# Kernel tuning notes

Hardware: AMD Instinct MI355X
Metric: run time of the kernel (lower is better)

Reference implementation:

```python
import jax, jax.numpy as jnp
import numpy as np

NUM_CLASSES = 151
EMBED = 200
HID = 512
OBJ_DIM = 4096
POS = 128
OBJ_IN = OBJ_DIM + EMBED + POS          # 4424
DEC_IN = HID + OBJ_IN                    # 4936
EDGE_IN = EMBED + HID + OBJ_DIM          # 4808
BN_EPS = 1e-5


def lstm_scan(xs, Wi, Wh, b):
    # xs: [T, D]; sequential chain LSTM (with_chain=True, chain_style='LSTM')
    H = Wh.shape[0]
    h0 = jnp.zeros((H,), xs.dtype)
    c0 = jnp.zeros((H,), xs.dtype)
    pre = xs @ Wi + b  # [T, 4H] hoist input projection out of the scan

    def step(carry, pt):
        h, c = carry
        g = pt + h @ Wh
        i, f, gg, o = jnp.split(g, 4)
        c = jax.nn.sigmoid(f) * c + jax.nn.sigmoid(i) * jnp.tanh(gg)
        h = jax.nn.sigmoid(o) * jnp.tanh(c)
        return (h, c), h

    _, hs = jax.lax.scan(step, (h0, c0), pre)
    return hs  # [T, H]


def setup_inputs() -> dict:
    key = jax.random.key(0)
    ks = jax.random.split(key, 24)
    s = 0.02
    N, B = 2048, 16
    inp = {
        "x": jax.random.normal(ks[0], (N, OBJ_DIM), jnp.float32),
        "obj_dists_in": jax.random.uniform(ks[1], (N, NUM_CLASSES), jnp.float32),
        "box_info": jax.random.uniform(ks[2], (N, 9), jnp.float32),
        "virtual_obj": jax.random.uniform(ks[3], (B, OBJ_IN), jnp.float32),
        "virtual_edge": jax.random.uniform(ks[4], (B, EDGE_IN), jnp.float32),
        # embeddings (GloVe-initialized in the original)
        "embed1": jax.random.normal(ks[5], (NUM_CLASSES, EMBED), jnp.float32) * s,
        "embed2": jax.random.normal(ks[6], (NUM_CLASSES, EMBED), jnp.float32) * s,
        # pos_embed MLP: Linear(9,32) -> BN(32) -> Linear(32,128) -> ReLU
        "pos_W1": jax.random.normal(ks[7], (9, 32), jnp.float32) * s,
        "pos_b1": jnp.zeros((32,), jnp.float32),
        "bn_gamma": jnp.ones((32,), jnp.float32),
        "bn_beta": jnp.zeros((32,), jnp.float32),
        "bn_mean": jnp.zeros((32,), jnp.float32),
        "bn_var": jnp.ones((32,), jnp.float32),
        "pos_W2": jax.random.normal(ks[8], (32, POS), jnp.float32) * s,
        "pos_b2": jnp.zeros((POS,), jnp.float32),
        # object context LSTM
        "obj_Wi": jax.random.normal(ks[9], (OBJ_IN, 4 * HID), jnp.float32) * s,
        "obj_Wh": jax.random.normal(ks[10], (HID, 4 * HID), jnp.float32) * s,
        "obj_b": jnp.zeros((4 * HID,), jnp.float32),
        # decoder tree-LSTM
        "dec_Wi": jax.random.normal(ks[11], (DEC_IN, 4 * HID), jnp.float32) * s,
        "dec_Wh": jax.random.normal(ks[12], (HID, 4 * HID), jnp.float32) * s,
        "dec_b": jnp.zeros((4 * HID,), jnp.float32),
        "out_W": jax.random.normal(ks[13], (HID, NUM_CLASSES), jnp.float32) * s,
        "out_b": jnp.zeros((NUM_CLASSES,), jnp.float32),
        # edge context LSTM
        "edge_Wi": jax.random.normal(ks[14], (EDGE_IN, 4 * HID), jnp.float32) * s,
        "edge_Wh": jax.random.normal(ks[15], (HID, 4 * HID), jnp.float32) * s,
        "edge_b": jnp.zeros((4 * HID,), jnp.float32),
    }
    return inp


def reference(x, obj_dists_in, box_info, virtual_obj, virtual_edge,
              embed1, embed2,
              pos_W1, pos_b1, bn_gamma, bn_beta, bn_mean, bn_var, pos_W2, pos_b2,
              obj_Wi, obj_Wh, obj_b,
              dec_Wi, dec_Wh, dec_b, out_W, out_b,
              edge_Wi, edge_Wh, edge_b):
    N = x.shape[0]
    B = virtual_obj.shape[0]
    # soft label embedding (sgdet/sgcls path): dists @ embed1.weight
    obj_embed = obj_dists_in @ embed1                      # [N, EMBED]
    # pos_embed MLP (BatchNorm in eval mode with running stats)
    h = box_info @ pos_W1 + pos_b1
    h = (h - bn_mean) * jax.lax.rsqrt(bn_var + BN_EPS) * bn_gamma + bn_beta
    pos_embed = jax.nn.relu(h @ pos_W2 + pos_b2)           # [N, POS]
    obj_pre_rep = jnp.concatenate([x, obj_embed, pos_embed], axis=-1)  # [N, OBJ_IN]

    # obj_ctx: append one virtual node per tree, chain tree-LSTM over the forest
    feats = jnp.concatenate([obj_pre_rep, virtual_obj], axis=0)        # [N+B, OBJ_IN]
    encoder_rep_full = lstm_scan(feats, obj_Wi, obj_Wh, obj_b)         # [N+B, HID]

    # decoder tree-LSTM: per-node recurrence + linear classification
    decoder_inp = jnp.concatenate([feats, encoder_rep_full], axis=1)   # [N+B, DEC_IN]
    dec_h = lstm_scan(decoder_inp, dec_Wi, dec_Wh, dec_b)              # [N+B, HID]
    dists_full = dec_h @ out_W + out_b                                 # [N+B, C]
    obj_dist = dists_full[:N]                    # strip virtual nodes ([:-B])
    obj_pred = jnp.argmax(obj_dist, axis=-1)     # commitments

    encoder_rep = encoder_rep_full[:N]

    # edge context: embed2 lookup on predicted labels + chain LSTM
    obj_embed2 = embed2[obj_pred]                                      # [N, EMBED]
    obj_rel_rep = jnp.concatenate([obj_embed2, x, encoder_rep], axis=-1)  # [N, EDGE_IN]
    edge_feats = jnp.concatenate([obj_rel_rep, virtual_edge], axis=0)
    edge_ctx = lstm_scan(edge_feats, edge_Wi, edge_Wh, edge_b)[:N]     # [N, HID]

    return obj_dist, obj_pred, edge_ctx
```

## Files before the change

### kernel.cpp

```cpp
#include <hip/hip_runtime.h>
#include <cstdint>
#include <cstddef>

#define N_OBJ 2048
#define NUM_CLASSES 151
#define EMBED 200
#define HID 512
#define OBJ_DIM 4096
#define POS 128
#define OBJ_IN 4424
#define EDGE_IN 4808
#define G4 2048
#define TSTEPS 2048
#define SPIN_FUSED 12000
#define OUT_PRED 309248
#define OUT_EDGE 311296

typedef unsigned long long ull;

__global__ void init_sync_kernel(unsigned* p, long n) {
  long i = blockIdx.x * (long)blockDim.x + threadIdx.x;
  long stride = (long)gridDim.x * blockDim.x;
  for (; i < n; i += stride) p[i] = 0u;
}

__global__ void obj_embed2_kernel(const float* __restrict__ dists,
                                  const float* __restrict__ embed1,
                                  float* __restrict__ objemb) {
  int r = blockIdx.x;
  __shared__ float drow[NUM_CLASSES];
  for (int c = threadIdx.x; c < NUM_CLASSES; c += blockDim.x)
    drow[c] = dists[(size_t)r * NUM_CLASSES + c];
  __syncthreads();
  for (int j = threadIdx.x; j < EMBED; j += blockDim.x) {
    float s = 0.f;
    for (int k = 0; k < NUM_CLASSES; ++k)
      s = fmaf(drow[k], embed1[(size_t)k * EMBED + j], s);
    objemb[(size_t)r * EMBED + j] = s;
  }
}

__global__ void pos2_kernel(const float* __restrict__ box,
                            const float* __restrict__ W1, const float* __restrict__ b1,
                            const float* __restrict__ gamma, const float* __restrict__ beta,
                            const float* __restrict__ mean, const float* __restrict__ var,
                            const float* __restrict__ W2, const float* __restrict__ b2,
                            float* __restrict__ posemb) {
  int r = blockIdx.x;
  __shared__ float h[32];
  __shared__ float bx[9];
  if (threadIdx.x < 9) bx[threadIdx.x] = box[(size_t)r * 9 + threadIdx.x];
  __syncthreads();
  if (threadIdx.x < 32) {
    float s = b1[threadIdx.x];
    for (int k = 0; k < 9; ++k) s = fmaf(bx[k], W1[k * 32 + threadIdx.x], s);
    s = (s - mean[threadIdx.x]) * (1.f / sqrtf(var[threadIdx.x] + 1e-5f)) * gamma[threadIdx.x]
        + beta[threadIdx.x];
    h[threadIdx.x] = s;
  }
  __syncthreads();
  int j = threadIdx.x;
  if (j < POS) {
    float s = b2[j];
    for (int k = 0; k < 32; ++k) s = fmaf(h[k], W2[k * POS + j], s);
    posemb[(size_t)r * POS + j] = fmaxf(s, 0.f);
  }
}

template <int ACC>
__global__ __launch_bounds__(256)
void gemm_kernel(const float* __restrict__ A, int lda,
                 const float* __restrict__ B, int ldb,
                 const float* __restrict__ bias,
                 float* __restrict__ C, int ldc,
                 int M, int N, int K) {
  __shared__ __align__(16) float As[16][68];
  __shared__ __align__(16) float Bs[16][64];
  const int row0 = blockIdx.y * 64;
  const int col0 = blockIdx.x * 64;
  const int tid = threadIdx.x;
  const int tx = tid & 15, ty = tid >> 4;
  float acc[4][4] = {};

  for (int k0 = 0; k0 < K; k0 += 16) {
#pragma unroll
    for (int l = 0; l < 4; ++l) {
      int idx = tid + l * 256;
      int m = idx >> 4, kk = idx & 15;
      int gm = row0 + m, gk = k0 + kk;
      As[kk][m] = (gm < M && gk < K) ? A[(size_t)gm * lda + gk] : 0.f;
    }
#pragma unroll
    for (int l = 0; l < 4; ++l) {
      int idx = tid + l * 256;
      int kk = idx >> 6, n = idx & 63;
      int gk = k0 + kk, gn = col0 + n;
      Bs[kk][n] = (gk < K && gn < N) ? B[(size_t)gk * ldb + gn] : 0.f;
    }
    __syncthreads();
#pragma unroll
    for (int kk = 0; kk < 16; ++kk) {
      float4 a = *reinterpret_cast<const float4*>(&As[kk][ty * 4]);
      float4 b = *reinterpret_cast<const float4*>(&Bs[kk][tx * 4]);
      acc[0][0] = fmaf(a.x, b.x, acc[0][0]); acc[0][1] = fmaf(a.x, b.y, acc[0][1]);
      acc[0][2] = fmaf(a.x, b.z, acc[0][2]); acc[0][3] = fmaf(a.x, b.w, acc[0][3]);
      acc[1][0] = fmaf(a.y, b.x, acc[1][0]); acc[1][1] = fmaf(a.y, b.y, acc[1][1]);
      acc[1][2] = fmaf(a.y, b.z, acc[1][2]); acc[1][3] = fmaf(a.y, b.w, acc[1][3]);
      acc[2][0] = fmaf(a.z, b.x, acc[2][0]); acc[2][1] = fmaf(a.z, b.y, acc[2][1]);
      acc[2][2] = fmaf(a.z, b.z, acc[2][2]); acc[2][3] = fmaf(a.z, b.w, acc[2][3]);
      acc[3][0] = fmaf(a.w, b.x, acc[3][0]); acc[3][1] = fmaf(a.w, b.y, acc[3][1]);
      acc[3][2] = fmaf(a.w, b.z, acc[3][2]); acc[3][3] = fmaf(a.w, b.w, acc[3][3]);
    }
    __syncthreads();
  }
#pragma unroll
  for (int i = 0; i < 4; ++i) {
    int gm = row0 + ty * 4 + i;
    if (gm >= M) continue;
#pragma unroll
    for (int j = 0; j < 4; ++j) {
      int gn = col0 + tx * 4 + j;
      if (gn >= N) continue;
      size_t o = (size_t)gm * ldc + gn;
      if (ACC) C[o] += acc[i][j];
      else C[o] = acc[i][j] + (bias ? bias[gn] : 0.f);
    }
  }
}

__device__ __forceinline__ void rec8_body(
    int blk, const float* __restrict__ pre, const float* __restrict__ Wh,
    const float* __restrict__ Wi2, ull* hXown, const ull* encXc,
    const ull* predX, const float* __restrict__ embT, float* outEdge,
    float4 (*w4)[32][64], float* hl, int* shPred) {
  const int tid = threadIdx.x;
  const int wv = tid >> 6;
  const int l = tid & 63;
  const int o = l & 7;
  const int c = l >> 3;
  const int gq = c & 3;
  const int dl = c >> 2;
  const int dim = blk * 8 + 2 * wv + dl;
  const int colw = gq * HID + dim;
  {
    const float* srcW = (o < 4) ? (Wh + (size_t)(o * 128) * G4 + colw)
                                : (Wi2 + (size_t)((o - 4) * 128) * G4 + colw);
#pragma unroll 4
    for (int j4 = 0; j4 < 32; ++j4) {
      float4 t;
      t.x = srcW[(size_t)(4 * j4 + 0) * G4];
      t.y = srcW[(size_t)(4 * j4 + 1) * G4];
      t.z = srcW[(size_t)(4 * j4 + 2) * G4];
      t.w = srcW[(size_t)(4 * j4 + 3) * G4];
      w4[wv][j4][l] = t;
    }
  }
  for (int i = tid; i < 1056; i += 256) hl[i] = 0.f;
  __syncthreads();

  float creg = 0.f;
  bool dead = false;
  for (int s = 0; s < TSTEPS; ++s) {
    float pre_v = pre[(size_t)s * G4 + colw];
    if (wv == 0) {
      const ull* srcE = encXc + (size_t)s * HID + l * 8;
      const ull* srcH = hXown + (size_t)(s - 1) * HID + l * 8;
      ull pe[8], ph[8], pp = 0;
      if (!dead) {
        int tries = 0;
        for (;;) {
          unsigned tE = 0xFFFFFFFFu, tH = 0xFFFFFFFFu, tP = 0xFFFFFFFFu;
#pragma unroll
          for (int j = 0; j < 8; ++j) {
            pe[j] = __hip_atomic_load(srcE + j, __ATOMIC_RELAXED, __HIP_MEMORY_SCOPE_AGENT);
            tE = min(tE, (unsigned)(pe[j] >> 32));
          }
          if (s > 0) {
#pragma unroll
            for (int j = 0; j < 8; ++j) {
              ph[j] = __hip_atomic_load(srcH + j, __ATOMIC_RELAXED, __HIP_MEMORY_SCOPE_AGENT);
              tH = min(tH, (unsigned)(ph[j] >> 32));
            }
          }
          if (predX) {
            pp = __hip_atomic_load(predX + s, __ATOMIC_RELAXED, __HIP_MEMORY_SCOPE_AGENT);
            tP = (unsigned)(pp >> 32);
          }
          bool ok = (tE >= (unsigned)(s + 1)) && (s == 0 || tH >= (unsigned)s) &&
                    (!predX || tP >= (unsigned)(s + 1));
          if (__all((int)ok)) break;
          if (++tries > SPIN_FUSED) { dead = true; break; }
          __builtin_amdgcn_s_sleep(2);
        }
      }
      if (dead) {
#pragma unroll
        for (int j = 0; j < 8; ++j) { pe[j] = 0ull; ph[j] = 0ull; }
        pp = 0;
      }
      const int ppH = 8 * l + 4 * (l >> 4);
      const int ppE = 528 + ppH;
      if (s > 0) {
#pragma unroll
        for (int j = 0; j < 8; ++j) hl[ppH + j] = __uint_as_float((unsigned)ph[j]);
      }
#pragma unroll
      for (int j = 0; j < 8; ++j) hl[ppE + j] = __uint_as_float((unsigned)pe[j]);
      if (predX && l == 0) *shPred = (int)(unsigned)(pp & 0xFFFFFFFFull);
    }
    __syncthreads();

    float emb = 0.f;
    if (embT) emb = embT[(size_t)(*shPred) * G4 + colw];

    float a0 = 0.f, a1 = 0.f, a2 = 0.f, a3 = 0.f;
    const float* hseg = &hl[132 * o];
#pragma unroll
    for (int j4 = 0; j4 < 32; ++j4) {
      float4 w = w4[wv][j4][l];
      float4 h4 = *reinterpret_cast<const float4*>(&hseg[4 * j4]);
      a0 = fmaf(w.x, h4.x, a0); a1 = fmaf(w.y, h4.y, a1);
      a2 = fmaf(w.z, h4.z, a2); a3 = fmaf(w.w, h4.w, a3);
    }
    float acc = (a0 + a1) + (a2 + a3);
    acc += __shfl_xor(acc, 1);
    acc += __shfl_xor(acc, 2);
    acc += __shfl_xor(acc, 4);
    float full = acc + pre_v + emb;
    int gb = dl * 32;
    float vi = __shfl(full, gb), vf = __shfl(full, gb + 8);
    float vg = __shfl(full, gb + 16), vo = __shfl(full, gb + 24);
    float si = 1.f / (1.f + __expf(-vi));
    float sf = 1.f / (1.f + __expf(-vf));
    float so = 1.f / (1.f + __expf(-vo));
    creg = sf * creg + si * tanhf(vg);
    float h = so * tanhf(creg);
    if ((l & 31) == 0) {
      if (outEdge) outEdge[(size_t)s * HID + dim] = h;
      ull pvs = ((ull)(unsigned)(s + 1) << 32) | (unsigned)__float_as_uint(h);
      __hip_atomic_store(hXown + (size_t)s * HID + dim, pvs, __ATOMIC_RELAXED,
                         __HIP_MEMORY_SCOPE_AGENT);
    }
  }
}

__global__ __launch_bounds__(256, 1)
void fused_all_kernel(const float* __restrict__ preO, const float* __restrict__ objWh,
                      const float* __restrict__ preD, const float* __restrict__ decWh,
                      const float* __restrict__ decWi2,
                      const float* __restrict__ epre, const float* __restrict__ embT,
                      const float* __restrict__ edgeWh, const float* __restrict__ edgeWi2,
                      const float* __restrict__ outW, const float* __restrict__ outB,
                      ull* encX, ull* dechX, ull* edgeX, ull* predX,
                      float* out) {
  __shared__ float4 w4[4][32][64];
  __shared__ float hl[1056];
  __shared__ int shPred;
  const int bid = blockIdx.x;
  const int tid = threadIdx.x;
  const int wv = tid >> 6;
  const int l = tid & 63;

  if (bid < 32) {
    const int q = l >> 2, qt = l & 3, dq = q >> 2, gq = q & 3;
    const int d0w = bid * 16 + wv * 4;
    const int colw = gq * HID + d0w + dq;
    {
      const float* base = objWh + (size_t)(qt * 128) * G4 + colw;
#pragma unroll 4
      for (int j4 = 0; j4 < 32; ++j4) {
        float4 t;
        t.x = base[(size_t)(4 * j4 + 0) * G4];
        t.y = base[(size_t)(4 * j4 + 1) * G4];
        t.z = base[(size_t)(4 * j4 + 2) * G4];
        t.w = base[(size_t)(4 * j4 + 3) * G4];
        w4[wv][j4][l] = t;
      }
    }
    for (int i = tid; i < 532; i += 256) hl[i] = 0.f;
    __syncthreads();

    float creg = 0.f;
    bool dead = false;
    for (int s = 0; s < TSTEPS; ++s) {
      float pre_v = preO[(size_t)s * G4 + colw];
      if (s > 0) {
        if (wv == 0) {
          const ull* src = encX + (size_t)(s - 1) * HID + l * 8;
          ull pv[8];
          if (!dead) {
            int tries = 0;
            for (;;) {
              unsigned tmin = 0xFFFFFFFFu;
#pragma unroll
              for (int j = 0; j < 8; ++j) {
                pv[j] = __hip_atomic_load(src + j, __ATOMIC_RELAXED, __HIP_MEMORY_SCOPE_AGENT);
                tmin = min(tmin, (unsigned)(pv[j] >> 32));
              }
              if (__all((int)(tmin >= (unsigned)s))) break;
              if (++tries > SPIN_FUSED) { dead = true; break; }
              __builtin_amdgcn_s_sleep(2);
            }
          }
          if (dead) {
#pragma unroll
            for (int j = 0; j < 8; ++j) pv[j] = 0ull;
          }
          const int pp = 8 * l + 4 * (l >> 4);
#pragma unroll
          for (int j = 0; j < 8; ++j) hl[pp + j] = __uint_as_float((unsigned)pv[j]);
        }
        __syncthreads();
      }
      float a0 = 0.f, a1 = 0.f, a2 = 0.f, a3 = 0.f;
      const float* hseg = &hl[132 * qt];
#pragma unroll
      for (int j4 = 0; j4 < 32; ++j4) {
        float4 w = w4[wv][j4][l];
        float4 h4 = *reinterpret_cast<const float4*>(&hseg[4 * j4]);
        a0 = fmaf(w.x, h4.x, a0); a1 = fmaf(w.y, h4.y, a1);
        a2 = fmaf(w.z, h4.z, a2); a3 = fmaf(w.w, h4.w, a3);
      }
      float acc = (a0 + a1) + (a2 + a3);
      acc += __shfl_xor(acc, 1);
      acc += __shfl_xor(acc, 2);
      float full = acc + pre_v;
      int gbase = (l & 48) | (l & 3);
      float vi = __shfl(full, gbase), vf = __shfl(full, gbase | 4);
      float vg = __shfl(full, gbase | 8), vo = __shfl(full, gbase | 12);
      float si = 1.f / (1.f + __expf(-vi));
      float sf = 1.f / (1.f + __expf(-vf));
      float so = 1.f / (1.f + __expf(-vo));
      creg = sf * creg + si * tanhf(vg);
      float h = so * tanhf(creg);
      if ((l & 15) == 0) {
        int dim = d0w + (l >> 4);
        ull pvs = ((ull)(unsigned)(s + 1) << 32) | (unsigned)__float_as_uint(h);
        __hip_atomic_store(encX + (size_t)s * HID + dim, pvs, __ATOMIC_RELAXED,
                           __HIP_MEMORY_SCOPE_AGENT);
      }
    }
  } else if (bid < 96) {
    rec8_body(bid - 32, preD, decWh, decWi2, dechX, encX,
              nullptr, nullptr, nullptr, w4, hl, &shPred);
  } else if (bid < 112) {
    const int a = bid - 96;
    float* dh = hl;
    float* lg = hl + 512;
    bool dead = false;
    for (int r = a; r < TSTEPS; r += 16) {
      if (wv == 0) {
        const ull* src = dechX + (size_t)r * HID + l * 8;
        ull pv[8];
        if (!dead) {
          int tries = 0;
          for (;;) {
            unsigned tmin = 0xFFFFFFFFu;
#pragma unroll
            for (int j = 0; j < 8; ++j) {
              pv[j] = __hip_atomic_load(src + j, __ATOMIC_RELAXED, __HIP_MEMORY_SCOPE_AGENT);
              tmin = min(tmin, (unsigned)(pv[j] >> 32));
            }
            if (__all((int)(tmin >= (unsigned)(r + 1)))) break;
            if (++tries > SPIN_FUSED) { dead = true; break; }
            __builtin_amdgcn_s_sleep(2);
          }
        }
        if (dead) {
#pragma unroll
          for (int j = 0; j < 8; ++j) pv[j] = 0ull;
        }
#pragma unroll
        for (int j = 0; j < 8; ++j) dh[l * 8 + j] = __uint_as_float((unsigned)pv[j]);
      }
      __syncthreads();
      if (tid < NUM_CLASSES) {
        float s2 = outB[tid];
#pragma unroll 8
        for (int k = 0; k < HID; ++k)
          s2 = fmaf(dh[k], outW[(size_t)k * NUM_CLASSES + tid], s2);
        lg[tid] = s2;
        out[(size_t)r * NUM_CLASSES + tid] = s2;
      }
      __syncthreads();
      if (wv == 0) {
        float bv = -3.4e38f;
        int bi = NUM_CLASSES;
        for (int cc = l; cc < NUM_CLASSES; cc += 64) {
          float v = lg[cc];
          if (v > bv) { bv = v; bi = cc; }
        }
        for (int off = 32; off; off >>= 1) {
          float ov = __shfl_xor(bv, off);
          int oi = __shfl_xor(bi, off);
          if (ov > bv || (ov == bv && oi < bi)) { bv = ov; bi = oi; }
        }
        if (l == 0) {
          out[OUT_PRED + r] = (float)bi;
          ull pvs = ((ull)(unsigned)(r + 1) << 32) | (unsigned)bi;
          __hip_atomic_store(predX + r, pvs, __ATOMIC_RELAXED, __HIP_MEMORY_SCOPE_AGENT);
        }
      }
      __syncthreads();
    }
  } else {
    rec8_body(bid - 112, epre, edgeWh, edgeWi2, edgeX, encX,
              predX, embT, out + OUT_EDGE, w4, hl, &shPred);
  }
}

extern "C" void kernel_launch(void* const* d_in, const int* in_sizes, int n_in,
                              void* d_out, int out_size, void* d_ws, size_t ws_size,
                              hipStream_t stream) {
  const float* x        = (const float*)d_in[0];
  const float* odists   = (const float*)d_in[1];
  const float* box      = (const float*)d_in[2];
  const float* embed1   = (const float*)d_in[5];
  const float* embed2   = (const float*)d_in[6];
  const float* pos_W1   = (const float*)d_in[7];
  const float* pos_b1   = (const float*)d_in[8];
  const float* bn_gamma = (const float*)d_in[9];
  const float* bn_beta  = (const float*)d_in[10];
  const float* bn_mean  = (const float*)d_in[11];
  const float* bn_var   = (const float*)d_in[12];
  const float* pos_W2   = (const float*)d_in[13];
  const float* pos_b2   = (const float*)d_in[14];
  const float* obj_Wi   = (const float*)d_in[15];
  const float* obj_Wh   = (const float*)d_in[16];
  const float* obj_b    = (const float*)d_in[17];
  const float* dec_Wi   = (const float*)d_in[18];
  const float* dec_Wh   = (const float*)d_in[19];
  const float* dec_b    = (const float*)d_in[20];
  const float* out_W    = (const float*)d_in[21];
  const float* out_b    = (const float*)d_in[22];
  const float* edge_Wi  = (const float*)d_in[23];
  const float* edge_Wh  = (const float*)d_in[24];
  const float* edge_b   = (const float*)d_in[25];

  float* out = (float*)d_out;

  float* preO   = (float*)d_ws;
  float* preD   = preO + (size_t)TSTEPS * G4;
  float* epre   = preD + (size_t)TSTEPS * G4;
  float* objemb = epre + (size_t)TSTEPS * G4;
  float* posemb = objemb + (size_t)TSTEPS * EMBED;
  float* embT   = posemb + (size_t)TSTEPS * POS;
  ull* encX  = (ull*)(embT + (size_t)NUM_CLASSES * G4);
  ull* dechX = encX + (size_t)TSTEPS * HID;
  ull* edgeX = dechX + (size_t)TSTEPS * HID;
  ull* predX = edgeX + (size_t)TSTEPS * HID;

  const size_t need_bytes =
      ((size_t)3 * TSTEPS * G4 + (size_t)TSTEPS * (EMBED + POS) +
       (size_t)NUM_CLASSES * G4) * 4 +
      ((size_t)3 * TSTEPS * HID + TSTEPS) * 8 + 256;
  if (ws_size < need_bytes) return;

  obj_embed2_kernel<<<TSTEPS, 256, 0, stream>>>(odists, embed1, objemb);
  pos2_kernel<<<TSTEPS, 128, 0, stream>>>(box, pos_W1, pos_b1, bn_gamma, bn_beta, bn_mean,
                                          bn_var, pos_W2, pos_b2, posemb);

  init_sync_kernel<<<2048, 256, 0, stream>>>((unsigned*)encX,
                                             ((long)3 * TSTEPS * HID + TSTEPS) * 2);

  gemm_kernel<0><<<dim3(32, 32), 256, 0, stream>>>(x, OBJ_DIM, obj_Wi, G4, obj_b,
                                                   preO, G4, TSTEPS, G4, OBJ_DIM);
  gemm_kernel<1><<<dim3(32, 32), 256, 0, stream>>>(objemb, EMBED, obj_Wi + (size_t)4096 * G4,
                                                   G4, nullptr, preO, G4, TSTEPS, G4, EMBED);
  gemm_kernel<1><<<dim3(32, 32), 256, 0, stream>>>(posemb, POS, obj_Wi + (size_t)4296 * G4,
                                                   G4, nullptr, preO, G4, TSTEPS, G4, POS);
  gemm_kernel<0><<<dim3(32, 32), 256, 0, stream>>>(x, OBJ_DIM, dec_Wi, G4, dec_b,
                                                   preD, G4, TSTEPS, G4, OBJ_DIM);
  gemm_kernel<1><<<dim3(32, 32), 256, 0, stream>>>(objemb, EMBED, dec_Wi + (size_t)4096 * G4,
                                                   G4, nullptr, preD, G4, TSTEPS, G4, EMBED);
  gemm_kernel<1><<<dim3(32, 32), 256, 0, stream>>>(posemb, POS, dec_Wi + (size_t)4296 * G4,
                                                   G4, nullptr, preD, G4, TSTEPS, G4, POS);
  gemm_kernel<0><<<dim3(32, 32), 256, 0, stream>>>(x, OBJ_DIM, edge_Wi + (size_t)200 * G4,
                                                   G4, edge_b, epre, G4, TSTEPS, G4, OBJ_DIM);
  gemm_kernel<0><<<dim3(32, 3), 256, 0, stream>>>(embed2, EMBED, edge_Wi, G4, nullptr,
                                                  embT, G4, NUM_CLASSES, G4, EMBED);

  fused_all_kernel<<<176, 256, 0, stream>>>(preO, obj_Wh, preD, dec_Wh,
                                            dec_Wi + (size_t)OBJ_IN * G4,
                                            epre, embT, edge_Wh,
                                            edge_Wi + (size_t)4296 * G4,
                                            out_W, out_b,
                                            encX, dechX, edgeX, predX, out);
}
```

Baseline: 9.896 ms.

## Use 64x128 GEMM tiles for large projections and split recurrence spin-waits

Adds a GEMM kernel with 64x128 output tiles and 4x8 accumulators per thread, and uses it for the three large K=4096 input projections. Larger tiles raise arithmetic intensity and cut global loads per FMA, at the cost of more registers and half as many blocks. Separately, the recurrence wait loop now polls the previous hidden state, the encoder state and the prediction flag in three sequential loops instead of one combined poll. This reduces redundant atomic reloads of already-ready data while spinning.

```diff
diff --git a/kernel.cpp b/kernel.cpp
--- a/kernel.cpp
+++ b/kernel.cpp
@@ -120,6 +120,76 @@
 #pragma unroll
     for (int j = 0; j < 4; ++j) {
       int gn = col0 + tx * 4 + j;
+      if (gn >= N) continue;
+      size_t o = (size_t)gm * ldc + gn;
+      if (ACC) C[o] += acc[i][j];
+      else C[o] = acc[i][j] + (bias ? bias[gn] : 0.f);
+    }
+  }
+}
+
+template <int ACC>
+__global__ __launch_bounds__(256)
+void gemm48_kernel(const float* __restrict__ A, int lda,
+                   const float* __restrict__ B, int ldb,
+                   const float* __restrict__ bias,
+                   float* __restrict__ C, int ldc,
+                   int M, int N, int K) {
+  __shared__ __align__(16) float As[16][68];
+  __shared__ __align__(16) float Bs[16][128];
+  const int row0 = blockIdx.y * 64;
+  const int col0 = blockIdx.x * 128;
+  const int tid = threadIdx.x;
+  const int tx = tid & 15, ty = tid >> 4;
+  float acc[4][8] = {};
+
+  for (int k0 = 0; k0 < K; k0 += 16) {
+#pragma unroll
+    for (int l = 0; l < 4; ++l) {
+      int idx = tid + l * 256;
+      int m = idx >> 4, kk = idx & 15;
+      int gm = row0 + m, gk = k0 + kk;
+      As[kk][m] = (gm < M && gk < K) ? A[(size_t)gm * lda + gk] : 0.f;
+    }
+#pragma unroll
+    for (int l = 0; l < 8; ++l) {
+      int idx = tid + l * 256;
+      int kk = idx >> 7, n = idx & 127;
+      int gk = k0 + kk, gn = col0 + n;
+      Bs[kk][n] = (gk < K && gn < N) ? B[(size_t)gk * ldb + gn] : 0.f;
+    }
+    __syncthreads();
+#pragma unroll
+    for (int kk = 0; kk < 16; ++kk) {
+      float4 a = *reinterpret_cast<const float4*>(&As[kk][ty * 4]);
+      float4 b0 = *reinterpret_cast<const float4*>(&Bs[kk][tx * 4]);
+      float4 b1 = *reinterpret_cast<const float4*>(&Bs[kk][64 + tx * 4]);
+      acc[0][0] = fmaf(a.x, b0.x, acc[0][0]); acc[0][1] = fmaf(a.x, b0.y, acc[0][1]);
+      acc[0][2] = fmaf(a.x, b0.z, acc[0][2]); acc[0][3] = fmaf(a.x, b0.w, acc[0][3]);
+      acc[0][4] = fmaf(a.x, b1.x, acc[0][4]); acc[0][5] = fmaf(a.x, b1.y, acc[0][5]);
+      acc[0][6] = fmaf(a.x, b1.z, acc[0][6]); acc[0][7] = fmaf(a.x, b1.w, acc[0][7]);
+      acc[1][0] = fmaf(a.y, b0.x, acc[1][0]); acc[1][1] = fmaf(a.y, b0.y, acc[1][1]);
+      acc[1][2] = fmaf(a.y, b0.z, acc[1][2]); acc[1][3] = fmaf(a.y, b0.w, acc[1][3]);
+      acc[1][4] = fmaf(a.y, b1.x, acc[1][4]); acc[1][5] = fmaf(a.y, b1.y, acc[1][5]);
+      acc[1][6] = fmaf(a.y, b1.z, acc[1][6]); acc[1][7] = fmaf(a.y, b1.w, acc[1][7]);
+      acc[2][0] = fmaf(a.z, b0.x, acc[2][0]); acc[2][1] = fmaf(a.z, b0.y, acc[2][1]);
+      acc[2][2] = fmaf(a.z, b0.z, acc[2][2]); acc[2][3] = fmaf(a.z, b0.w, acc[2][3]);
+      acc[2][4] = fmaf(a.z, b1.x, acc[2][4]); acc[2][5] = fmaf(a.z, b1.y, acc[2][5]);
+      acc[2][6] = fmaf(a.z, b1.z, acc[2][6]); acc[2][7] = fmaf(a.z, b1.w, acc[2][7]);
+      acc[3][0] = fmaf(a.w, b0.x, acc[3][0]); acc[3][1] = fmaf(a.w, b0.y, acc[3][1]);
+      acc[3][2] = fmaf(a.w, b0.z, acc[3][2]); acc[3][3] = fmaf(a.w, b0.w, acc[3][3]);
+      acc[3][4] = fmaf(a.w, b1.x, acc[3][4]); acc[3][5] = fmaf(a.w, b1.y, acc[3][5]);
+      acc[3][6] = fmaf(a.w, b1.z, acc[3][6]); acc[3][7] = fmaf(a.w, b1.w, acc[3][7]);
+    }
+    __syncthreads();
+  }
+#pragma unroll
+  for (int i = 0; i < 4; ++i) {
+    int gm = row0 + ty * 4 + i;
+    if (gm >= M) continue;
+#pragma unroll
+    for (int j = 0; j < 8; ++j) {
+      int gn = col0 + ((j < 4) ? (tx * 4 + j) : (64 + tx * 4 + j - 4));
       if (gn >= N) continue;
       size_t o = (size_t)gm * ldc + gn;
       if (ACC) C[o] += acc[i][j];
@@ -166,29 +236,39 @@
       const ull* srcE = encXc + (size_t)s * HID + l * 8;
       const ull* srcH = hXown + (size_t)(s - 1) * HID + l * 8;
       ull pe[8], ph[8], pp = 0;
+      if (!dead && s > 0) {
+        int tries = 0;
+        for (;;) {
+          unsigned tH = 0xFFFFFFFFu;
+#pragma unroll
+          for (int j = 0; j < 8; ++j) {
+            ph[j] = __hip_atomic_load(srcH + j, __ATOMIC_RELAXED, __HIP_MEMORY_SCOPE_AGENT);
+            tH = min(tH, (unsigned)(ph[j] >> 32));
+          }
+          if (__all((int)(tH >= (unsigned)s))) break;
+          if (++tries > SPIN_FUSED) { dead = true; break; }
+          __builtin_amdgcn_s_sleep(2);
+        }
+      }
       if (!dead) {
         int tries = 0;
         for (;;) {
-          unsigned tE = 0xFFFFFFFFu, tH = 0xFFFFFFFFu, tP = 0xFFFFFFFFu;
+          unsigned tE = 0xFFFFFFFFu;
 #pragma unroll
           for (int j = 0; j < 8; ++j) {
             pe[j] = __hip_atomic_load(srcE + j, __ATOMIC_RELAXED, __HIP_MEMORY_SCOPE_AGENT);
             tE = min(tE, (unsigned)(pe[j] >> 32));
           }
-          if (s > 0) {
-#pragma unroll
-            for (int j = 0; j < 8; ++j) {
-              ph[j] = __hip_atomic_load(srcH + j, __ATOMIC_RELAXED, __HIP_MEMORY_SCOPE_AGENT);
-              tH = min(tH, (unsigned)(ph[j] >> 32));
-            }
-          }
-          if (predX) {
-            pp = __hip_atomic_load(predX + s, __ATOMIC_RELAXED, __HIP_MEMORY_SCOPE_AGENT);
-            tP = (unsigned)(pp >> 32);
-          }
-          bool ok = (tE >= (unsigned)(s + 1)) && (s == 0 || tH >= (unsigned)s) &&
-                    (!predX || tP >= (unsigned)(s + 1));
-          if (__all((int)ok)) break;
+          if (__all((int)(tE >= (unsigned)(s + 1)))) break;
+          if (++tries > SPIN_FUSED) { dead = true; break; }
+          __builtin_amdgcn_s_sleep(2);
+        }
+      }
+      if (!dead && predX) {
+        int tries = 0;
+        for (;;) {
+          pp = __hip_atomic_load(predX + s, __ATOMIC_RELAXED, __HIP_MEMORY_SCOPE_AGENT);
+          if (__all((int)((unsigned)(pp >> 32) >= (unsigned)(s + 1)))) break;
           if (++tries > SPIN_FUSED) { dead = true; break; }
           __builtin_amdgcn_s_sleep(2);
         }
@@ -463,20 +543,20 @@
   init_sync_kernel<<<2048, 256, 0, stream>>>((unsigned*)encX,
                                              ((long)3 * TSTEPS * HID + TSTEPS) * 2);
 
-  gemm_kernel<0><<<dim3(32, 32), 256, 0, stream>>>(x, OBJ_DIM, obj_Wi, G4, obj_b,
-                                                   preO, G4, TSTEPS, G4, OBJ_DIM);
+  gemm48_kernel<0><<<dim3(16, 32), 256, 0, stream>>>(x, OBJ_DIM, obj_Wi, G4, obj_b,
+                                                     preO, G4, TSTEPS, G4, OBJ_DIM);
   gemm_kernel<1><<<dim3(32, 32), 256, 0, stream>>>(objemb, EMBED, obj_Wi + (size_t)4096 * G4,
                                                    G4, nullptr, preO, G4, TSTEPS, G4, EMBED);
   gemm_kernel<1><<<dim3(32, 32), 256, 0, stream>>>(posemb, POS, obj_Wi + (size_t)4296 * G4,
                                                    G4, nullptr, preO, G4, TSTEPS, G4, POS);
-  gemm_kernel<0><<<dim3(32, 32), 256, 0, stream>>>(x, OBJ_DIM, dec_Wi, G4, dec_b,
-                                                   preD, G4, TSTEPS, G4, OBJ_DIM);
+  gemm48_kernel<0><<<dim3(16, 32), 256, 0, stream>>>(x, OBJ_DIM, dec_Wi, G4, dec_b,
+                                                     preD, G4, TSTEPS, G4, OBJ_DIM);
   gemm_kernel<1><<<dim3(32, 32), 256, 0, stream>>>(objemb, EMBED, dec_Wi + (size_t)4096 * G4,
                                                    G4, nullptr, preD, G4, TSTEPS, G4, EMBED);
   gemm_kernel<1><<<dim3(32, 32), 256, 0, stream>>>(posemb, POS, dec_Wi + (size_t)4296 * G4,
                                                    G4, nullptr, preD, G4, TSTEPS, G4, POS);
-  gemm_kernel<0><<<dim3(32, 32), 256, 0, stream>>>(x, OBJ_DIM, edge_Wi + (size_t)200 * G4,
-                                                   G4, edge_b, epre, G4, TSTEPS, G4, OBJ_DIM);
+  gemm48_kernel<0><<<dim3(16, 32), 256, 0, stream>>>(x, OBJ_DIM, edge_Wi + (size_t)200 * G4,
+                                                     G4, edge_b, epre, G4, TSTEPS, G4, OBJ_DIM);
   gemm_kernel<0><<<dim3(32, 3), 256, 0, stream>>>(embed2, EMBED, edge_Wi, G4, nullptr,
                                                   embT, G4, NUM_CLASSES, G4, EMBED);
 
```

Result: slower. 12.07 ms (+22.0%).
